# Kernel optimization log

Hardware: AMD Instinct MI355X
Metric: run time of the kernel (lower is better)

## Reference

```python
import jax, jax.numpy as jnp
import numpy as np

N_NODES = 50000
N_EDGES = 800000
IN_FEATS = 128
OUT_FEATS = 128


def setup_inputs() -> dict:
    key = jax.random.key(0)
    k1, k2, k3, k4, k5, k6 = jax.random.split(key, 6)
    features = jax.random.normal(k1, (N_NODES, IN_FEATS), dtype=jnp.float32)
    norm = jax.random.uniform(k2, (N_NODES, 1), dtype=jnp.float32)
    W = jax.random.normal(k3, (OUT_FEATS, IN_FEATS), dtype=jnp.float32) * (1.0 / np.sqrt(IN_FEATS))
    b = jax.random.normal(k4, (OUT_FEATS,), dtype=jnp.float32) * 0.01
    src = jax.random.randint(k5, (N_EDGES,), 0, N_NODES, dtype=jnp.int32)
    dst = jax.random.randint(k6, (N_EDGES,), 0, N_NODES, dtype=jnp.int32)
    return {"features": features, "norm": norm, "W": W, "b": b, "src": src, "dst": dst}


def reference(features, norm, W, b, src, dst):
    # message: h_src * norm_src  -> [E, F]
    msg = features[src] * norm[src]
    # reduce: sum over incoming edges, scale by dst norm -> [N, F]
    agg = jax.ops.segment_sum(msg, dst, num_segments=N_NODES) * norm
    # node apply: linear + tanh
    h = jnp.tanh(agg @ W.T + b)
    return h
```

## Files before the change

### kernel.cpp

```cpp
#include <hip/hip_runtime.h>
#include <hip/hip_fp16.h>
#include <math.h>

#define NBITS 7
#define BNODES 128
#define CHUNK 4096
#define BSHIFT 12

typedef _Float16 half4v __attribute__((ext_vector_type(4)));
typedef _Float16 half8v __attribute__((ext_vector_type(8)));
typedef float f32x4 __attribute__((ext_vector_type(4)));

__device__ __forceinline__ unsigned hpack(float a, float b) {
  __half2 h = __floats2half2_rn(a, b);
  return *reinterpret_cast<unsigned*>(&h);
}

union GemmSmem {
  struct {
    _Float16 Wh[128][136];
    _Float16 Ah[64][136];
  } s;
  float Cs[64][132];
};

__global__ __launch_bounds__(256) void gemm_kernel(
    const float* __restrict__ feat, const float* __restrict__ norm,
    const float* __restrict__ W, unsigned* __restrict__ Yh, int n_nodes,
    int* __restrict__ cursor, int nb) {
  __shared__ __align__(16) GemmSmem sm;
  const int t = threadIdx.x;
  const int node0 = blockIdx.x * 64;

  if (blockIdx.x == 0) {
    for (int i = t; i < nb; i += 256) cursor[i] = 0;
  }

#pragma unroll
  for (int k = 0; k < 16; ++k) {
    int e4 = k * 256 + t;
    int oo = e4 >> 5;
    int f4 = (e4 & 31) * 4;
    float4 w = *(const float4*)&W[oo * 128 + f4];
    half4v h;
    h.x = (_Float16)w.x; h.y = (_Float16)w.y;
    h.z = (_Float16)w.z; h.w = (_Float16)w.w;
    *(half4v*)&sm.s.Wh[oo][f4] = h;
  }
#pragma unroll
  for (int k = 0; k < 8; ++k) {
    int e4 = k * 256 + t;
    int nn = e4 >> 5;
    int f4 = (e4 & 31) * 4;
    int node = node0 + nn;
    float4 a = (node < n_nodes)
                   ? *(const float4*)&feat[(size_t)node * 128 + f4]
                   : make_float4(0.f, 0.f, 0.f, 0.f);
    half4v h;
    h.x = (_Float16)a.x; h.y = (_Float16)a.y;
    h.z = (_Float16)a.z; h.w = (_Float16)a.w;
    *(half4v*)&sm.s.Ah[nn][f4] = h;
  }
  __syncthreads();

  const int wv = t >> 6;
  const int l = t & 63;
  const int row16 = l & 15;
  const int kq = l >> 4;

  f32x4 acc[8];
#pragma unroll
  for (int nt = 0; nt < 8; ++nt) acc[nt] = (f32x4){0.f, 0.f, 0.f, 0.f};

#pragma unroll
  for (int ks = 0; ks < 4; ++ks) {
    half8v afrag = *(const half8v*)&sm.s.Ah[wv * 16 + row16][kq * 8 + ks * 32];
#pragma unroll
    for (int nt = 0; nt < 8; ++nt) {
      half8v bfrag = *(const half8v*)&sm.s.Wh[nt * 16 + row16][kq * 8 + ks * 32];
      acc[nt] = __builtin_amdgcn_mfma_f32_16x16x32_f16(afrag, bfrag, acc[nt], 0, 0, 0);
    }
  }
  __syncthreads();

#pragma unroll
  for (int nt = 0; nt < 8; ++nt)
#pragma unroll
    for (int r = 0; r < 4; ++r)
      sm.Cs[wv * 16 + kq * 4 + r][nt * 16 + row16] = acc[nt][r];
  __syncthreads();

#pragma unroll
  for (int k = 0; k < 8; ++k) {
    int p = k * 256 + t;
    int nn = p >> 5;
    int q = p & 31;
    int node = node0 + nn;
    if (node < n_nodes) {
      float nm = norm[node];
      float4 v = *(float4*)&sm.Cs[nn][q * 4];
      uint2 u;
      u.x = hpack(v.x * nm, v.y * nm);
      u.y = hpack(v.z * nm, v.w * nm);
      ((uint2*)Yh)[(size_t)node * 32 + q] = u;
    }
  }
}

__global__ __launch_bounds__(256) void partition_kernel(
    const int* __restrict__ src, const int* __restrict__ dst,
    int* __restrict__ cursor, unsigned* __restrict__ recs, int n_edges, int nb) {
  __shared__ int lcount[512];
  __shared__ int lbase[512];
  __shared__ int gbase[512];
  __shared__ int aux[256];
  __shared__ unsigned stage[CHUNK];
  __shared__ int s_total;
  const int t = threadIdx.x;
  const int cbase = blockIdx.x * CHUNK;

  lcount[t] = 0; lcount[t + 256] = 0;
  __syncthreads();

  int es[16], ed[16], rk[16];
#pragma unroll
  for (int q = 0; q < 4; ++q) {
    int i4 = (cbase >> 2) + q * 256 + t;
    int e0 = i4 << 2;
    int4 sv, dv;
    if (e0 + 3 < n_edges) {
      sv = ((const int4*)src)[i4];
      dv = ((const int4*)dst)[i4];
    } else {
      sv.x = (e0 + 0 < n_edges) ? src[e0 + 0] : 0;
      sv.y = (e0 + 1 < n_edges) ? src[e0 + 1] : 0;
      sv.z = (e0 + 2 < n_edges) ? src[e0 + 2] : 0;
      sv.w = 0;
      dv.x = (e0 + 0 < n_edges) ? dst[e0 + 0] : -1;
      dv.y = (e0 + 1 < n_edges) ? dst[e0 + 1] : -1;
      dv.z = (e0 + 2 < n_edges) ? dst[e0 + 2] : -1;
      dv.w = -1;
    }
    es[q * 4 + 0] = sv.x; ed[q * 4 + 0] = dv.x;
    es[q * 4 + 1] = sv.y; ed[q * 4 + 1] = dv.y;
    es[q * 4 + 2] = sv.z; ed[q * 4 + 2] = dv.z;
    es[q * 4 + 3] = sv.w; ed[q * 4 + 3] = dv.w;
  }
#pragma unroll
  for (int k = 0; k < 16; ++k)
    rk[k] = (ed[k] >= 0) ? atomicAdd(&lcount[ed[k] >> NBITS], 1) : 0;
  __syncthreads();

  int a = lcount[2 * t] + lcount[2 * t + 1];
  aux[t] = a;
  __syncthreads();
  for (int off = 1; off < 256; off <<= 1) {
    int u = (t >= off) ? aux[t - off] : 0;
    __syncthreads();
    aux[t] += u;
    __syncthreads();
  }
  int ex = aux[t] - a;
  lbase[2 * t] = ex;
  lbase[2 * t + 1] = ex + lcount[2 * t];
  if (t == 255) s_total = aux[255];
  __syncthreads();

  for (int b = t; b < nb; b += 256)
    gbase[b] = (lcount[b] > 0) ? ((b << BSHIFT) + atomicAdd(&cursor[b], lcount[b]))
                               : 0;
  __syncthreads();

#pragma unroll
  for (int k = 0; k < 16; ++k) {
    if (ed[k] >= 0) {
      int b = ed[k] >> NBITS;
      stage[lbase[b] + rk[k]] = (unsigned)es[k] | ((unsigned)ed[k] << 16);
    }
  }
  __syncthreads();

  int total = s_total;
  for (int r = t; r < total; r += 256) {
    unsigned rec = stage[r];
    int b = (int)(rec >> (16 + NBITS));
    recs[gbase[b] + (r - lbase[b])] = rec;
  }
}

__global__ __launch_bounds__(256) void localize_kernel(
    const unsigned* __restrict__ recs, const int* __restrict__ cursor,
    int* __restrict__ sorted_src, int* __restrict__ row_start,
    int* __restrict__ counts_d, int n_nodes) {
  __shared__ int lc[BNODES];
  __shared__ int ls[BNODES];
  __shared__ int cur[BNODES];
  const int t = threadIdx.x;
  const int b = blockIdx.x;
  const int cbeg = b << BSHIFT;
  const int cnt = cursor[b];

  if (t < BNODES) lc[t] = 0;
  __syncthreads();
  for (int i = t; i < cnt; i += 256) {
    unsigned rec = recs[cbeg + i];
    atomicAdd(&lc[(rec >> 16) & (BNODES - 1)], 1);
  }
  __syncthreads();
  if (t < BNODES) ls[t] = lc[t];
  __syncthreads();
  for (int off = 1; off < BNODES; off <<= 1) {
    int u = (t < BNODES && t >= off) ? ls[t - off] : 0;
    __syncthreads();
    if (t < BNODES) ls[t] += u;
    __syncthreads();
  }
  if (t < BNODES) {
    int ex = ls[t] - lc[t];
    cur[t] = ex;
    int node = (b << NBITS) + t;
    if (node < n_nodes) {
      counts_d[node] = lc[t];
      row_start[node] = cbeg + ex;
    }
  }
  __syncthreads();
  for (int i = t; i < cnt; i += 256) {
    unsigned rec = recs[cbeg + i];
    int nl = (rec >> 16) & (BNODES - 1);
    int p = atomicAdd(&cur[nl], 1);
    sorted_src[cbeg + p] = (int)(rec & 0xffffu);
  }
}

__global__ __launch_bounds__(256) void gather_kernel(
    const unsigned* __restrict__ Yh, const int* __restrict__ sorted_src,
    const int* __restrict__ row_start, const int* __restrict__ counts_d,
    const float* __restrict__ norm, const float* __restrict__ b,
    float* __restrict__ out, int n_nodes) {
  int node = blockIdx.x * 4 + (threadIdx.x >> 6);
  if (node >= n_nodes) return;
  int lane = threadIdx.x & 63;
  int beg = row_start[node];
  int cnt = counts_d[node];
  float accx = 0.f, accy = 0.f;

  for (int base = 0; base < cnt; base += 64) {
    int m = cnt - base;
    if (m > 64) m = 64;
    int myid = (lane < m) ? sorted_src[beg + base + lane] : 0;
    int g = 0;
    for (; g + 8 <= m; g += 8) {
      int s0 = __builtin_amdgcn_readlane(myid, g + 0);
      int s1 = __builtin_amdgcn_readlane(myid, g + 1);
      int s2 = __builtin_amdgcn_readlane(myid, g + 2);
      int s3 = __builtin_amdgcn_readlane(myid, g + 3);
      int s4 = __builtin_amdgcn_readlane(myid, g + 4);
      int s5 = __builtin_amdgcn_readlane(myid, g + 5);
      int s6 = __builtin_amdgcn_readlane(myid, g + 6);
      int s7 = __builtin_amdgcn_readlane(myid, g + 7);
      unsigned u0 = Yh[(size_t)s0 * 64 + lane];
      unsigned u1 = Yh[(size_t)s1 * 64 + lane];
      unsigned u2 = Yh[(size_t)s2 * 64 + lane];
      unsigned u3 = Yh[(size_t)s3 * 64 + lane];
      unsigned u4 = Yh[(size_t)s4 * 64 + lane];
      unsigned u5 = Yh[(size_t)s5 * 64 + lane];
      unsigned u6 = Yh[(size_t)s6 * 64 + lane];
      unsigned u7 = Yh[(size_t)s7 * 64 + lane];
      float2 v0 = __half22float2(*reinterpret_cast<__half2*>(&u0));
      float2 v1 = __half22float2(*reinterpret_cast<__half2*>(&u1));
      float2 v2 = __half22float2(*reinterpret_cast<__half2*>(&u2));
      float2 v3 = __half22float2(*reinterpret_cast<__half2*>(&u3));
      float2 v4 = __half22float2(*reinterpret_cast<__half2*>(&u4));
      float2 v5 = __half22float2(*reinterpret_cast<__half2*>(&u5));
      float2 v6 = __half22float2(*reinterpret_cast<__half2*>(&u6));
      float2 v7 = __half22float2(*reinterpret_cast<__half2*>(&u7));
      accx += (v0.x + v1.x) + (v2.x + v3.x) + ((v4.x + v5.x) + (v6.x + v7.x));
      accy += (v0.y + v1.y) + (v2.y + v3.y) + ((v4.y + v5.y) + (v6.y + v7.y));
    }
    for (; g < m; ++g) {
      int s = __builtin_amdgcn_readlane(myid, g);
      unsigned u = Yh[(size_t)s * 64 + lane];
      float2 v = __half22float2(*reinterpret_cast<__half2*>(&u));
      accx += v.x;
      accy += v.y;
    }
  }
  float nm = norm[node];
  float2 bb = ((const float2*)b)[lane];
  float2 h;
  h.x = tanhf(accx * nm + bb.x);
  h.y = tanhf(accy * nm + bb.y);
  ((float2*)out)[(size_t)node * 64 + lane] = h;
}

extern "C" void kernel_launch(void* const* d_in, const int* in_sizes, int n_in,
                              void* d_out, int out_size, void* d_ws, size_t ws_size,
                              hipStream_t stream) {
  const float* feat = (const float*)d_in[0];
  const float* norm = (const float*)d_in[1];
  const float* W    = (const float*)d_in[2];
  const float* b    = (const float*)d_in[3];
  const int* src    = (const int*)d_in[4];
  const int* dst    = (const int*)d_in[5];
  float* out        = (float*)d_out;

  const int n_nodes = in_sizes[1];
  const int n_edges = in_sizes[4];
  const int nb = (n_nodes + BNODES - 1) / BNODES;

  char* base = (char*)d_ws;
  unsigned* Yh = (unsigned*)base;
  size_t off = (size_t)n_nodes * 64 * sizeof(unsigned);
  off = (off + 255) & ~(size_t)255;
  int* cursor = (int*)(base + off); off += (size_t)nb * 4;
  off = (off + 255) & ~(size_t)255;
  unsigned* recs = (unsigned*)(base + off); off += ((size_t)nb << BSHIFT) * 4;
  off = (off + 255) & ~(size_t)255;
  int* sorted_src = (int*)(base + off); off += ((size_t)nb << BSHIFT) * 4;
  off = (off + 255) & ~(size_t)255;
  int* row_start = (int*)(base + off); off += (size_t)n_nodes * 4;
  off = (off + 255) & ~(size_t)255;
  int* counts_d = (int*)(base + off); off += (size_t)n_nodes * 4;

  int gblocks = (n_nodes + 63) / 64;
  gemm_kernel<<<gblocks, 256, 0, stream>>>(feat, norm, W, Yh, n_nodes, cursor, nb);

  int chunks = (n_edges + CHUNK - 1) / CHUNK;
  partition_kernel<<<chunks, 256, 0, stream>>>(src, dst, cursor, recs, n_edges, nb);

  localize_kernel<<<nb, 256, 0, stream>>>(recs, cursor, sorted_src,
                                          row_start, counts_d, n_nodes);

  int nblocks = (n_nodes + 3) / 4;
  gather_kernel<<<nblocks, 256, 0, stream>>>(Yh, sorted_src, row_start, counts_d,
                                             norm, b, out, n_nodes);
}
```

Before: 75.34 us.

## Write GEMM output straight from MFMA registers, widen localize blocks, unroll gather deeper

The GEMM swaps the MFMA operand order so each lane holds four consecutive output features for one node. It then scales by norm and stores fp16 straight from registers, dropping the shared-memory C staging, two barriers and the union layout. The localize kernel launches with 512 threads instead of 256, and the gather adds a 16-wide unrolled load batch ahead of the 8-wide loop to keep more loads in flight. Risks are less coalesced 8-byte GEMM stores and higher register pressure in the gather, which may lower occupancy.

```diff
diff --git a/kernel.cpp b/kernel.cpp
--- a/kernel.cpp
+++ b/kernel.cpp
@@ -16,19 +16,12 @@
   return *reinterpret_cast<unsigned*>(&h);
 }
 
-union GemmSmem {
-  struct {
-    _Float16 Wh[128][136];
-    _Float16 Ah[64][136];
-  } s;
-  float Cs[64][132];
-};
-
 __global__ __launch_bounds__(256) void gemm_kernel(
     const float* __restrict__ feat, const float* __restrict__ norm,
     const float* __restrict__ W, unsigned* __restrict__ Yh, int n_nodes,
     int* __restrict__ cursor, int nb) {
-  __shared__ __align__(16) GemmSmem sm;
+  __shared__ __align__(16) _Float16 Wh[128][136];
+  __shared__ __align__(16) _Float16 Ah[64][136];
   const int t = threadIdx.x;
   const int node0 = blockIdx.x * 64;
 
@@ -45,7 +38,7 @@
     half4v h;
     h.x = (_Float16)w.x; h.y = (_Float16)w.y;
     h.z = (_Float16)w.z; h.w = (_Float16)w.w;
-    *(half4v*)&sm.s.Wh[oo][f4] = h;
+    *(half4v*)&Wh[oo][f4] = h;
   }
 #pragma unroll
   for (int k = 0; k < 8; ++k) {
@@ -59,7 +52,7 @@
     half4v h;
     h.x = (_Float16)a.x; h.y = (_Float16)a.y;
     h.z = (_Float16)a.z; h.w = (_Float16)a.w;
-    *(half4v*)&sm.s.Ah[nn][f4] = h;
+    *(half4v*)&Ah[nn][f4] = h;
   }
   __syncthreads();
 
@@ -70,39 +63,27 @@
 
   f32x4 acc[8];
 #pragma unroll
-  for (int nt = 0; nt < 8; ++nt) acc[nt] = (f32x4){0.f, 0.f, 0.f, 0.f};
+  for (int ot = 0; ot < 8; ++ot) acc[ot] = (f32x4){0.f, 0.f, 0.f, 0.f};
 
 #pragma unroll
   for (int ks = 0; ks < 4; ++ks) {
-    half8v afrag = *(const half8v*)&sm.s.Ah[wv * 16 + row16][kq * 8 + ks * 32];
-#pragma unroll
-    for (int nt = 0; nt < 8; ++nt) {
-      half8v bfrag = *(const half8v*)&sm.s.Wh[nt * 16 + row16][kq * 8 + ks * 32];
-      acc[nt] = __builtin_amdgcn_mfma_f32_16x16x32_f16(afrag, bfrag, acc[nt], 0, 0, 0);
-    }
-  }
-  __syncthreads();
-
-#pragma unroll
-  for (int nt = 0; nt < 8; ++nt)
-#pragma unroll
-    for (int r = 0; r < 4; ++r)
-      sm.Cs[wv * 16 + kq * 4 + r][nt * 16 + row16] = acc[nt][r];
-  __syncthreads();
-
-#pragma unroll
-  for (int k = 0; k < 8; ++k) {
-    int p = k * 256 + t;
-    int nn = p >> 5;
-    int q = p & 31;
-    int node = node0 + nn;
-    if (node < n_nodes) {
-      float nm = norm[node];
-      float4 v = *(float4*)&sm.Cs[nn][q * 4];
+    half8v nfrag = *(const half8v*)&Ah[wv * 16 + row16][kq * 8 + ks * 32];
+#pragma unroll
+    for (int ot = 0; ot < 8; ++ot) {
+      half8v wfrag = *(const half8v*)&Wh[ot * 16 + row16][kq * 8 + ks * 32];
+      acc[ot] = __builtin_amdgcn_mfma_f32_16x16x32_f16(wfrag, nfrag, acc[ot], 0, 0, 0);
+    }
+  }
+
+  int node = node0 + wv * 16 + row16;
+  if (node < n_nodes) {
+    float nm = norm[node];
+#pragma unroll
+    for (int ot = 0; ot < 8; ++ot) {
       uint2 u;
-      u.x = hpack(v.x * nm, v.y * nm);
-      u.y = hpack(v.z * nm, v.w * nm);
-      ((uint2*)Yh)[(size_t)node * 32 + q] = u;
+      u.x = hpack(acc[ot][0] * nm, acc[ot][1] * nm);
+      u.y = hpack(acc[ot][2] * nm, acc[ot][3] * nm);
+      ((uint2*)Yh)[(size_t)node * 32 + ot * 4 + kq] = u;
     }
   }
 }
@@ -188,7 +169,7 @@
   }
 }
 
-__global__ __launch_bounds__(256) void localize_kernel(
+__global__ __launch_bounds__(512) void localize_kernel(
     const unsigned* __restrict__ recs, const int* __restrict__ cursor,
     int* __restrict__ sorted_src, int* __restrict__ row_start,
     int* __restrict__ counts_d, int n_nodes) {
@@ -202,7 +183,7 @@
 
   if (t < BNODES) lc[t] = 0;
   __syncthreads();
-  for (int i = t; i < cnt; i += 256) {
+  for (int i = t; i < cnt; i += 512) {
     unsigned rec = recs[cbeg + i];
     atomicAdd(&lc[(rec >> 16) & (BNODES - 1)], 1);
   }
@@ -225,7 +206,7 @@
     }
   }
   __syncthreads();
-  for (int i = t; i < cnt; i += 256) {
+  for (int i = t; i < cnt; i += 512) {
     unsigned rec = recs[cbeg + i];
     int nl = (rec >> 16) & (BNODES - 1);
     int p = atomicAdd(&cur[nl], 1);
@@ -250,33 +231,33 @@
     if (m > 64) m = 64;
     int myid = (lane < m) ? sorted_src[beg + base + lane] : 0;
     int g = 0;
+    for (; g + 16 <= m; g += 16) {
+      int sid[16];
+      unsigned uu[16];
+#pragma unroll
+      for (int q = 0; q < 16; ++q) sid[q] = __builtin_amdgcn_readlane(myid, g + q);
+#pragma unroll
+      for (int q = 0; q < 16; ++q) uu[q] = Yh[(size_t)sid[q] * 64 + lane];
+#pragma unroll
+      for (int q = 0; q < 16; ++q) {
+        float2 v = __half22float2(*reinterpret_cast<__half2*>(&uu[q]));
+        accx += v.x;
+        accy += v.y;
+      }
+    }
     for (; g + 8 <= m; g += 8) {
-      int s0 = __builtin_amdgcn_readlane(myid, g + 0);
-      int s1 = __builtin_amdgcn_readlane(myid, g + 1);
-      int s2 = __builtin_amdgcn_readlane(myid, g + 2);
-      int s3 = __builtin_amdgcn_readlane(myid, g + 3);
-      int s4 = __builtin_amdgcn_readlane(myid, g + 4);
-      int s5 = __builtin_amdgcn_readlane(myid, g + 5);
-      int s6 = __builtin_amdgcn_readlane(myid, g + 6);
-      int s7 = __builtin_amdgcn_readlane(myid, g + 7);
-      unsigned u0 = Yh[(size_t)s0 * 64 + lane];
-      unsigned u1 = Yh[(size_t)s1 * 64 + lane];
-      unsigned u2 = Yh[(size_t)s2 * 64 + lane];
-      unsigned u3 = Yh[(size_t)s3 * 64 + lane];
-      unsigned u4 = Yh[(size_t)s4 * 64 + lane];
-      unsigned u5 = Yh[(size_t)s5 * 64 + lane];
-      unsigned u6 = Yh[(size_t)s6 * 64 + lane];
-      unsigned u7 = Yh[(size_t)s7 * 64 + lane];
-      float2 v0 = __half22float2(*reinterpret_cast<__half2*>(&u0));
-      float2 v1 = __half22float2(*reinterpret_cast<__half2*>(&u1));
-      float2 v2 = __half22float2(*reinterpret_cast<__half2*>(&u2));
-      float2 v3 = __half22float2(*reinterpret_cast<__half2*>(&u3));
-      float2 v4 = __half22float2(*reinterpret_cast<__half2*>(&u4));
-      float2 v5 = __half22float2(*reinterpret_cast<__half2*>(&u5));
-      float2 v6 = __half22float2(*reinterpret_cast<__half2*>(&u6));
-      float2 v7 = __half22float2(*reinterpret_cast<__half2*>(&u7));
-      accx += (v0.x + v1.x) + (v2.x + v3.x) + ((v4.x + v5.x) + (v6.x + v7.x));
-      accy += (v0.y + v1.y) + (v2.y + v3.y) + ((v4.y + v5.y) + (v6.y + v7.y));
+      int sid[8];
+      unsigned uu[8];
+#pragma unroll
+      for (int q = 0; q < 8; ++q) sid[q] = __builtin_amdgcn_readlane(myid, g + q);
+#pragma unroll
+      for (int q = 0; q < 8; ++q) uu[q] = Yh[(size_t)sid[q] * 64 + lane];
+#pragma unroll
+      for (int q = 0; q < 8; ++q) {
+        float2 v = __half22float2(*reinterpret_cast<__half2*>(&uu[q]));
+        accx += v.x;
+        accy += v.y;
+      }
     }
     for (; g < m; ++g) {
       int s = __builtin_amdgcn_readlane(myid, g);
@@ -329,7 +310,7 @@
   int chunks = (n_edges + CHUNK - 1) / CHUNK;
   partition_kernel<<<chunks, 256, 0, stream>>>(src, dst, cursor, recs, n_edges, nb);
 
-  localize_kernel<<<nb, 256, 0, stream>>>(recs, cursor, sorted_src,
+  localize_kernel<<<nb, 512, 0, stream>>>(recs, cursor, sorted_src,
                                           row_start, counts_d, n_nodes);
 
   int nblocks = (n_nodes + 3) / 4;
```

After: 74.47 us. Within noise of the previous version (-1.2%).
